# Kernel tuning notes

Hardware: AMD Instinct MI355X
Metric: run time of the kernel (lower is better)

The kernel has to match this reference:

```python
import jax, jax.numpy as jnp
import numpy as np

H = 4            # attention heads
N = 50000        # num nodes
E = 800000       # num edges
IN, HID, OUT = 256, 32, 32
NEG_SLOPE = 0.2  # DGL GATConv default leaky_relu slope


def setup_inputs() -> dict:
    key = jax.random.key(0)
    ks = jax.random.split(key, 16)
    x = jax.random.normal(ks[0], (N, IN), jnp.float32)
    src = jax.random.randint(ks[1], (E,), 0, N, dtype=jnp.int32)
    dst = jax.random.randint(ks[2], (E,), 0, N, dtype=jnp.int32)

    def lin(k, a, b):
        return jax.random.normal(k, (a, b), jnp.float32) * (1.0 / np.sqrt(a))

    def attn(k, d):
        return jax.random.normal(k, (H, d), jnp.float32) * 0.1

    HW = H * HID
    return {
        "x": x, "src": src, "dst": dst,
        "W1": lin(ks[3], IN, HW), "al1": attn(ks[4], HID), "ar1": attn(ks[5], HID), "b1": jnp.zeros((H, HID), jnp.float32),
        "W2": lin(ks[6], HW, HW), "al2": attn(ks[7], HID), "ar2": attn(ks[8], HID), "b2": jnp.zeros((H, HID), jnp.float32),
        "W3": lin(ks[9], HW, H * OUT), "al3": attn(ks[10], OUT), "ar3": attn(ks[11], OUT), "b3": jnp.zeros((H, OUT), jnp.float32),
    }


def gat_layer(x, W, al, ar, b, src, dst, act):
    # x: [N, F_in]; W: [F_in, H*D]; al/ar/b: [H, D]
    n = x.shape[0]
    d = al.shape[1]
    h = (x @ W).reshape(n, H, d)                         # [N, H, D]
    el = jnp.sum(h * al, axis=-1)                        # [N, H]
    er = jnp.sum(h * ar, axis=-1)                        # [N, H]
    e = jax.nn.leaky_relu(el[src] + er[dst], NEG_SLOPE)  # [E, H] edge scores
    # segment softmax over incoming edges of each dst node
    m = jax.ops.segment_max(e, dst, num_segments=n)      # [N, H]
    m = jnp.where(jnp.isfinite(m), m, 0.0)               # empty segments -> -inf
    ex = jnp.exp(e - m[dst])                             # [E, H]
    s = jax.ops.segment_sum(ex, dst, num_segments=n)     # [N, H]
    alpha = ex / s[dst]                                  # [E, H]
    out = jax.ops.segment_sum(h[src] * alpha[:, :, None], dst, num_segments=n)  # [N, H, D]
    out = out + b
    return act(out) if act is not None else out


def reference(x, src, dst, W1, al1, ar1, b1, W2, al2, ar2, b2, W3, al3, ar3, b3):
    h = gat_layer(x, W1, al1, ar1, b1, src, dst, jax.nn.relu).reshape(N, -1)   # flatten heads
    h = gat_layer(h, W2, al2, ar2, b2, src, dst, jax.nn.elu).reshape(N, -1)    # flatten heads
    h = gat_layer(h, W3, al3, ar3, b3, src, dst, None).mean(axis=1)            # mean over heads
    return h
```

## Files before the change

### kernel.cpp

```cpp
#include <hip/hip_runtime.h>
#include <hip/hip_bf16.h>
#include <hip/hip_fp16.h>
#include <stdint.h>

#define NNODES 50000
#define NEDGES 800000
#define HEADS 4
#define DSTRIDE 64

#define GEMM_GRID ((NNODES + 127) / 128)
#define B2_GROUPS 8
#define B2_PER_GROUP 256
#define NODES_PER_GROUP (NNODES / B2_GROUPS)

typedef __attribute__((ext_vector_type(8))) short bf16x8;
typedef __attribute__((ext_vector_type(4))) float f32x4;

union frag_u { uint32_t u[4]; bf16x8 v; uint4 q; };

__device__ __forceinline__ float lrelu(float x) { return x > 0.f ? x : 0.2f * x; }

__device__ __forceinline__ uint32_t pack_bf16(float a, float b) {
  __hip_bfloat162 t{__float2bfloat16(a), __float2bfloat16(b)};
  return *reinterpret_cast<uint32_t*>(&t);
}

__device__ __forceinline__ void split8(const float4& x0, const float4& x1,
                                       frag_u& hi, frag_u& lo) {
  float f[8] = {x0.x, x0.y, x0.z, x0.w, x1.x, x1.y, x1.z, x1.w};
#pragma unroll
  for (int p = 0; p < 4; ++p) {
    uint32_t ua = __float_as_uint(f[2 * p]);
    uint32_t ub = __float_as_uint(f[2 * p + 1]);
    hi.u[p] = (ua >> 16) | (ub & 0xffff0000u);
    float ra = f[2 * p] - __uint_as_float(ua & 0xffff0000u);
    float rb = f[2 * p + 1] - __uint_as_float(ub & 0xffff0000u);
    lo.u[p] = (__float_as_uint(ra) >> 16) | (__float_as_uint(rb) & 0xffff0000u);
  }
}

__global__ __launch_bounds__(256) void k_build2(const int* __restrict__ src,
                                                const int* __restrict__ dst,
                                                int* __restrict__ cnt,
                                                unsigned short* __restrict__ esrc) {
  int g = blockIdx.x & (B2_GROUPS - 1);
  int sub = blockIdx.x >> 3;
  int lo = g * NODES_PER_GROUP, hi = lo + NODES_PER_GROUP;
  const int tstride = B2_PER_GROUP * 256 * 8;
  for (int e = (sub * 256 + threadIdx.x) * 8; e < NEDGES; e += tstride) {
    int4 da = *(const int4*)&dst[e];
    int4 db = *(const int4*)&dst[e + 4];
#pragma unroll
    for (int q = 0; q < 8; ++q) {
      int d = q < 4 ? (q == 0 ? da.x : q == 1 ? da.y : q == 2 ? da.z : da.w)
                    : (q == 4 ? db.x : q == 5 ? db.y : q == 6 ? db.z : db.w);
      if (d >= lo && d < hi) {
        int r = atomicAdd(&cnt[d], 1);
        if (r < DSTRIDE) esrc[(size_t)d * DSTRIDE + r] = (unsigned short)src[e + q];
      }
    }
  }
}

__device__ __forceinline__ void splitw_one(const float* __restrict__ W, int t_local,
                                           uint4* __restrict__ WPh, uint4* __restrict__ WPl) {
  int lane = t_local & 63;
  int ct = (t_local >> 6) & 7;
  int ks = t_local >> 9;
  int lg = lane >> 4, lm = lane & 15;
  int n = ct * 16 + lm;
  frag_u hi, lo;
#pragma unroll
  for (int p = 0; p < 4; ++p) {
    float a = W[(size_t)(ks * 32 + lg * 8 + 2 * p) * 128 + n];
    float b = W[(size_t)(ks * 32 + lg * 8 + 2 * p + 1) * 128 + n];
    uint32_t ua = __float_as_uint(a), ub = __float_as_uint(b);
    hi.u[p] = (ua >> 16) | (ub & 0xffff0000u);
    float ra = a - __uint_as_float(ua & 0xffff0000u);
    float rb = b - __uint_as_float(ub & 0xffff0000u);
    lo.u[p] = (__float_as_uint(ra) >> 16) | (__float_as_uint(rb) & 0xffff0000u);
  }
  WPh[t_local] = hi.q;
  WPl[t_local] = lo.q;
}

__global__ void k_splitw_all(const float* __restrict__ W1, const float* __restrict__ W2,
                             const float* __restrict__ W3,
                             uint4* __restrict__ WPh1, uint4* __restrict__ WPl1,
                             uint4* __restrict__ WPh2, uint4* __restrict__ WPl2,
                             uint4* __restrict__ WPh3, uint4* __restrict__ WPl3,
                             int* __restrict__ cnt) {
  int t = blockIdx.x * blockDim.x + threadIdx.x;
  for (int i = t; i < NNODES; i += 32 * 256) cnt[i] = 0;
  int ks = t >> 9;
  if (ks < 8)        splitw_one(W1, t,            WPh1, WPl1);
  else if (ks < 12)  splitw_one(W2, t - 8 * 512,  WPh2, WPl2);
  else if (ks < 16)  splitw_one(W3, t - 12 * 512, WPh3, WPl3);
}

template <int K, int XBF>
__global__ __launch_bounds__(256) void k_gemm_mfma(
    const void* __restrict__ Xv, const uint4* __restrict__ WPh,
    const uint4* __restrict__ WPl, const float* __restrict__ al,
    const float* __restrict__ ar, uint32_t* __restrict__ Hb,
    float* __restrict__ el, float* __restrict__ er, int nrows) {
  __shared__ uint4 lph[512];
  __shared__ uint4 lpl[512];
  const int tid = threadIdx.x;
  const int wv = tid >> 6;
  const int lane = tid & 63;
  const int lm = lane & 15;
  const int lg = lane >> 4;
  const int rbase = blockIdx.x * 128 + wv * 32;

  int grow0 = rbase + lm;
  int grow1 = rbase + 16 + lm;
  int lrow0 = min(grow0, nrows - 1);
  int lrow1 = min(grow1, nrows - 1);

  const float* xp0 = nullptr;
  const float* xp1 = nullptr;
  const uint32_t* xq0 = nullptr;
  const uint32_t* xq1 = nullptr;
  if (XBF) {
    xq0 = (const uint32_t*)Xv + (size_t)lrow0 * 64 + lg * 4;
    xq1 = (const uint32_t*)Xv + (size_t)lrow1 * 64 + lg * 4;
  } else {
    xp0 = (const float*)Xv + (size_t)lrow0 * K + lg * 8;
    xp1 = (const float*)Xv + (size_t)lrow1 * K + lg * 8;
  }

  f32x4 acc[2][8];
#pragma unroll
  for (int rt = 0; rt < 2; ++rt)
#pragma unroll
    for (int ct = 0; ct < 8; ++ct) acc[rt][ct] = f32x4{0.f, 0.f, 0.f, 0.f};

  for (int ks = 0; ks < K / 32; ++ks) {
    frag_u xh0, xl0, xh1, xl1;
    if (XBF) {
      xh0.q = *(const uint4*)(xq0 + ks * 16);
      xh1.q = *(const uint4*)(xq1 + ks * 16);
    } else {
      float4 a0 = *(const float4*)(xp0 + ks * 32);
      float4 a1 = *(const float4*)(xp0 + ks * 32 + 4);
      float4 b0 = *(const float4*)(xp1 + ks * 32);
      float4 b1 = *(const float4*)(xp1 + ks * 32 + 4);
      split8(a0, a1, xh0, xl0);
      split8(b0, b1, xh1, xl1);
    }
    lph[tid]       = WPh[(size_t)ks * 512 + tid];
    lph[tid + 256] = WPh[(size_t)ks * 512 + 256 + tid];
    lpl[tid]       = WPl[(size_t)ks * 512 + tid];
    lpl[tid + 256] = WPl[(size_t)ks * 512 + 256 + tid];
    __syncthreads();
#pragma unroll
    for (int ct = 0; ct < 8; ++ct) {
      frag_u bh, bl;
      bh.q = lph[ct * 64 + lane];
      bl.q = lpl[ct * 64 + lane];
      if (XBF) {
        acc[0][ct] = __builtin_amdgcn_mfma_f32_16x16x32_bf16(bh.v, xh0.v, acc[0][ct], 0, 0, 0);
        acc[0][ct] = __builtin_amdgcn_mfma_f32_16x16x32_bf16(bl.v, xh0.v, acc[0][ct], 0, 0, 0);
        acc[1][ct] = __builtin_amdgcn_mfma_f32_16x16x32_bf16(bh.v, xh1.v, acc[1][ct], 0, 0, 0);
        acc[1][ct] = __builtin_amdgcn_mfma_f32_16x16x32_bf16(bl.v, xh1.v, acc[1][ct], 0, 0, 0);
      } else {
        acc[0][ct] = __builtin_amdgcn_mfma_f32_16x16x32_bf16(bh.v, xh0.v, acc[0][ct], 0, 0, 0);
        acc[0][ct] = __builtin_amdgcn_mfma_f32_16x16x32_bf16(bl.v, xh0.v, acc[0][ct], 0, 0, 0);
        acc[0][ct] = __builtin_amdgcn_mfma_f32_16x16x32_bf16(bh.v, xl0.v, acc[0][ct], 0, 0, 0);
        acc[1][ct] = __builtin_amdgcn_mfma_f32_16x16x32_bf16(bh.v, xh1.v, acc[1][ct], 0, 0, 0);
        acc[1][ct] = __builtin_amdgcn_mfma_f32_16x16x32_bf16(bl.v, xh1.v, acc[1][ct], 0, 0, 0);
        acc[1][ct] = __builtin_amdgcn_mfma_f32_16x16x32_bf16(bh.v, xl1.v, acc[1][ct], 0, 0, 0);
      }
    }
    __syncthreads();
  }

#pragma unroll
  for (int rt = 0; rt < 2; ++rt) {
    int grow = rt ? grow1 : grow0;
    float pe[4] = {0.f, 0.f, 0.f, 0.f};
    float pr[4] = {0.f, 0.f, 0.f, 0.f};
#pragma unroll
    for (int ct = 0; ct < 8; ++ct) {
      int h = ct >> 1;
      int dc = (ct & 1) * 16 + lg * 4;
      float4 a4 = *(const float4*)&al[h * 32 + dc];
      float4 r4 = *(const float4*)&ar[h * 32 + dc];
      f32x4 c = acc[rt][ct];
      pe[h] += c[0] * a4.x + c[1] * a4.y + c[2] * a4.z + c[3] * a4.w;
      pr[h] += c[0] * r4.x + c[1] * r4.y + c[2] * r4.z + c[3] * r4.w;
    }
#pragma unroll
    for (int i = 0; i < 4; ++i) {
      pe[i] += __shfl_xor(pe[i], 16); pe[i] += __shfl_xor(pe[i], 32);
      pr[i] += __shfl_xor(pr[i], 16); pr[i] += __shfl_xor(pr[i], 32);
    }
    if (grow < nrows) {
#pragma unroll
      for (int ct = 0; ct < 8; ++ct) {
        f32x4 c = acc[rt][ct];
        uint2 st{pack_bf16(c[0], c[1]), pack_bf16(c[2], c[3])};
        *(uint2*)&Hb[(size_t)grow * 64 + ct * 8 + lg * 2] = st;
      }
      if (lg == 0) {
        *(float4*)&el[(size_t)grow * 4] = float4{pe[0], pe[1], pe[2], pe[3]};
        *(float4*)&er[(size_t)grow * 4] = float4{pr[0], pr[1], pr[2], pr[3]};
      }
    }
  }
}

template <int MODE>
__global__ __launch_bounds__(256) void k_agg(const uint32_t* __restrict__ Hb,
                                             const float* __restrict__ el,
                                             const float* __restrict__ er,
                                             const int* __restrict__ deg_,
                                             const unsigned short* __restrict__ esrc,
                                             const float* __restrict__ B,
                                             void* __restrict__ outp) {
  int gt = blockIdx.x * blockDim.x + threadIdx.x;
  int v = gt >> 6;
  int lane = gt & 63;
  if (v >= NNODES) return;
  int deg = min(deg_[v], DSTRIDE);
  int h = lane >> 4;
  int e16 = lane & 15;
  float erh = er[(size_t)v * 4 + h];
  const int vbase = v * DSTRIDE;

  float den = 0.f, acc0 = 0.f, acc1 = 0.f;
  for (int base = 0; base < deg; base += 16) {
    uint32_t pk = 0;
    if (base + e16 < deg) {
      int u = esrc[vbase + base + e16];
      float ex1 = __expf(lrelu(el[(size_t)u * 4 + h] + erh));
      den += ex1;
      pk = ((uint32_t)u << 16) | (uint32_t)__half_as_ushort(__float2half(ex1));
    }
    uint32_t hw[16];
    float w[16];
#pragma unroll
    for (int j = 0; j < 16; ++j) {
      int srcl = (lane & 48) | j;
      uint32_t pkj = __shfl(pk, srcl);
      w[j] = __half2float(__ushort_as_half((unsigned short)(pkj & 0xffffu)));
      hw[j] = Hb[(size_t)(pkj >> 16) * 64 + lane];
    }
#pragma unroll
    for (int j = 0; j < 16; ++j) {
      acc0 += w[j] * __uint_as_float(hw[j] << 16);
      acc1 += w[j] * __uint_as_float(hw[j] & 0xffff0000u);
    }
  }
#pragma unroll
  for (int s = 1; s < 16; s <<= 1) den += __shfl_xor(den, s);
  float inv = den > 0.f ? 1.f / den : 0.f;

  int d = (2 * lane) & 31;
  float v0 = acc0 * inv + B[h * 32 + d];
  float v1 = acc1 * inv + B[h * 32 + d + 1];

  if (MODE == 0) {
    ((uint32_t*)outp)[(size_t)v * 64 + lane] = pack_bf16(fmaxf(v0, 0.f), fmaxf(v1, 0.f));
  } else if (MODE == 1) {
    float a0 = v0 > 0.f ? v0 : expm1f(v0);
    float a1 = v1 > 0.f ? v1 : expm1f(v1);
    ((uint32_t*)outp)[(size_t)v * 64 + lane] = pack_bf16(a0, a1);
  } else {
    float t0 = v0, t1 = v1;
    t0 += __shfl_xor(t0, 16); t0 += __shfl_xor(t0, 32);
    t1 += __shfl_xor(t1, 16); t1 += __shfl_xor(t1, 32);
    if (lane < 16) {
      float2 o{t0 * 0.25f, t1 * 0.25f};
      *(float2*)((float*)outp + (size_t)v * 32 + 2 * lane) = o;
    }
  }
}

extern "C" void kernel_launch(void* const* d_in, const int* in_sizes, int n_in,
                              void* d_out, int out_size, void* d_ws, size_t ws_size,
                              hipStream_t stream) {
  const float* x   = (const float*)d_in[0];
  const int* src   = (const int*)d_in[1];
  const int* dst   = (const int*)d_in[2];
  const float* W1  = (const float*)d_in[3];
  const float* al1 = (const float*)d_in[4];
  const float* ar1 = (const float*)d_in[5];
  const float* b1  = (const float*)d_in[6];
  const float* W2  = (const float*)d_in[7];
  const float* al2 = (const float*)d_in[8];
  const float* ar2 = (const float*)d_in[9];
  const float* b2  = (const float*)d_in[10];
  const float* W3  = (const float*)d_in[11];
  const float* al3 = (const float*)d_in[12];
  const float* ar3 = (const float*)d_in[13];
  const float* b3  = (const float*)d_in[14];

  uint8_t* p = (uint8_t*)d_ws;
  auto alloc = [&](size_t bytes) {
    uint8_t* r = p;
    p += (bytes + 255) & ~(size_t)255;
    return r;
  };
  uint32_t* Hb          = (uint32_t*)alloc((size_t)NNODES * 64 * 4);
  uint32_t* Ab          = (uint32_t*)alloc((size_t)NNODES * 64 * 4);
  float* el             = (float*)alloc((size_t)NNODES * 4 * 4);
  float* er             = (float*)alloc((size_t)NNODES * 4 * 4);
  int* cnt              = (int*)alloc((size_t)NNODES * 4);
  unsigned short* esrc  = (unsigned short*)alloc((size_t)NNODES * DSTRIDE * 2);
  uint4* WPh1           = (uint4*)alloc((size_t)256 * 16 * 16);
  uint4* WPl1           = (uint4*)alloc((size_t)256 * 16 * 16);
  uint4* WPh2           = (uint4*)alloc((size_t)128 * 16 * 16);
  uint4* WPl2           = (uint4*)alloc((size_t)128 * 16 * 16);
  uint4* WPh3           = (uint4*)alloc((size_t)128 * 16 * 16);
  uint4* WPl3           = (uint4*)alloc((size_t)128 * 16 * 16);

  k_splitw_all<<<32, 256, 0, stream>>>(W1, W2, W3, WPh1, WPl1, WPh2, WPl2,
                                       WPh3, WPl3, cnt);
  k_build2<<<B2_GROUPS * B2_PER_GROUP, 256, 0, stream>>>(src, dst, cnt, esrc);

  const int agg_grid = (NNODES * 64 + 255) / 256;

  k_gemm_mfma<256, 0><<<GEMM_GRID, 256, 0, stream>>>(x, WPh1, WPl1, al1, ar1, Hb, el, er, NNODES);
  k_agg<0><<<agg_grid, 256, 0, stream>>>(Hb, el, er, cnt, esrc, b1, Ab);

  k_gemm_mfma<128, 1><<<GEMM_GRID, 256, 0, stream>>>(Ab, WPh2, WPl2, al2, ar2, Hb, el, er, NNODES);
  k_agg<1><<<agg_grid, 256, 0, stream>>>(Hb, el, er, cnt, esrc, b2, Ab);

  k_gemm_mfma<128, 1><<<GEMM_GRID, 256, 0, stream>>>(Ab, WPh3, WPl3, al3, ar3, Hb, el, er, NNODES);
  k_agg<2><<<agg_grid, 256, 0, stream>>>(Hb, el, er, cnt, esrc, b3, d_out);
}
```

Baseline: 215.1 us.

## Replace group-filtered edge scan with two-pass bucket partition for CSR build

The adjacency build used to scan every edge eight times, once per destination-node group, so each group's atomics stayed localized. It now runs a single bucketing pass that packs (local dst, src) into 32-bit entries and appends them to per-group buckets, using shared-memory counts and one global atomic per block per group. A second kernel then scatters each bucket into the per-node esrc slots. This removes the repeated full reads of dst, but adds an intermediate buffer with a fixed capacity per group that could overflow on skewed inputs, and an extra kernel launch.

```diff
diff --git a/kernel.cpp b/kernel.cpp
--- a/kernel.cpp
+++ b/kernel.cpp
@@ -9,9 +9,10 @@
 #define DSTRIDE 64
 
 #define GEMM_GRID ((NNODES + 127) / 128)
-#define B2_GROUPS 8
-#define B2_PER_GROUP 256
-#define NODES_PER_GROUP (NNODES / B2_GROUPS)
+#define NGROUPS 8
+#define GROUP_SHIFT 13
+#define BUCK_CAP 163840
+#define SC2_BPG 128
 
 typedef __attribute__((ext_vector_type(8))) short bf16x8;
 typedef __attribute__((ext_vector_type(4))) float f32x4;
@@ -39,25 +40,61 @@
   }
 }
 
-__global__ __launch_bounds__(256) void k_build2(const int* __restrict__ src,
+__global__ __launch_bounds__(256) void k_bucket(const int* __restrict__ src,
                                                 const int* __restrict__ dst,
-                                                int* __restrict__ cnt,
-                                                unsigned short* __restrict__ esrc) {
-  int g = blockIdx.x & (B2_GROUPS - 1);
+                                                int* __restrict__ bcnt,
+                                                uint32_t* __restrict__ bucket) {
+  __shared__ int lcnt[NGROUPS], lbase[NGROUPS];
+  if (threadIdx.x < NGROUPS) lcnt[threadIdx.x] = 0;
+  __syncthreads();
+  int e0 = (blockIdx.x * 256 + threadIdx.x) * 4;
+  int g[4], rank[4];
+  uint32_t entry[4];
+  int4 d4, s4;
+  if (e0 < NEDGES) {
+    d4 = *(const int4*)&dst[e0];
+    s4 = *(const int4*)&src[e0];
+  }
+#pragma unroll
+  for (int q = 0; q < 4; ++q) {
+    if (e0 < NEDGES) {
+      int d = q == 0 ? d4.x : q == 1 ? d4.y : q == 2 ? d4.z : d4.w;
+      int s = q == 0 ? s4.x : q == 1 ? s4.y : q == 2 ? s4.z : s4.w;
+      g[q] = d >> GROUP_SHIFT;
+      entry[q] = ((uint32_t)(d & ((1 << GROUP_SHIFT) - 1)) << 16) | (uint32_t)s;
+      rank[q] = atomicAdd(&lcnt[g[q]], 1);
+    } else {
+      g[q] = -1;
+    }
+  }
+  __syncthreads();
+  if (threadIdx.x < NGROUPS && lcnt[threadIdx.x] > 0)
+    lbase[threadIdx.x] = atomicAdd(&bcnt[threadIdx.x], lcnt[threadIdx.x]);
+  __syncthreads();
+#pragma unroll
+  for (int q = 0; q < 4; ++q) {
+    if (g[q] >= 0) {
+      uint32_t pos = (uint32_t)(lbase[g[q]] + rank[q]);
+      if (pos < BUCK_CAP) bucket[(size_t)g[q] * BUCK_CAP + pos] = entry[q];
+    }
+  }
+}
+
+__global__ __launch_bounds__(256) void k_scatter2(const int* __restrict__ bcnt,
+                                                  const uint32_t* __restrict__ bucket,
+                                                  int* __restrict__ cnt,
+                                                  unsigned short* __restrict__ esrc) {
+  int g = blockIdx.x & (NGROUPS - 1);
   int sub = blockIdx.x >> 3;
-  int lo = g * NODES_PER_GROUP, hi = lo + NODES_PER_GROUP;
-  const int tstride = B2_PER_GROUP * 256 * 8;
-  for (int e = (sub * 256 + threadIdx.x) * 8; e < NEDGES; e += tstride) {
-    int4 da = *(const int4*)&dst[e];
-    int4 db = *(const int4*)&dst[e + 4];
-#pragma unroll
-    for (int q = 0; q < 8; ++q) {
-      int d = q < 4 ? (q == 0 ? da.x : q == 1 ? da.y : q == 2 ? da.z : da.w)
-                    : (q == 4 ? db.x : q == 5 ? db.y : q == 6 ? db.z : db.w);
-      if (d >= lo && d < hi) {
-        int r = atomicAdd(&cnt[d], 1);
-        if (r < DSTRIDE) esrc[(size_t)d * DSTRIDE + r] = (unsigned short)src[e + q];
-      }
+  int n = min(bcnt[g], BUCK_CAP);
+  const uint32_t* bk = bucket + (size_t)g * BUCK_CAP;
+  int gbase = g << GROUP_SHIFT;
+  for (int i = sub * 256 + threadIdx.x; i < n; i += SC2_BPG * 256) {
+    uint32_t ent = bk[i];
+    int d = gbase + (int)(ent >> 16);
+    if (d < NNODES) {
+      int r = atomicAdd(&cnt[d], 1);
+      if (r < DSTRIDE) esrc[(size_t)d * DSTRIDE + r] = (unsigned short)(ent & 0xffffu);
     }
   }
 }
@@ -89,9 +126,10 @@
                              uint4* __restrict__ WPh1, uint4* __restrict__ WPl1,
                              uint4* __restrict__ WPh2, uint4* __restrict__ WPl2,
                              uint4* __restrict__ WPh3, uint4* __restrict__ WPl3,
-                             int* __restrict__ cnt) {
+                             int* __restrict__ cnt, int* __restrict__ bcnt) {
   int t = blockIdx.x * blockDim.x + threadIdx.x;
   for (int i = t; i < NNODES; i += 32 * 256) cnt[i] = 0;
+  if (t < NGROUPS) bcnt[t] = 0;
   int ks = t >> 9;
   if (ks < 8)        splitw_one(W1, t,            WPh1, WPl1);
   else if (ks < 12)  splitw_one(W2, t - 8 * 512,  WPh2, WPl2);
@@ -309,6 +347,8 @@
   float* er             = (float*)alloc((size_t)NNODES * 4 * 4);
   int* cnt              = (int*)alloc((size_t)NNODES * 4);
   unsigned short* esrc  = (unsigned short*)alloc((size_t)NNODES * DSTRIDE * 2);
+  int* bcnt             = (int*)alloc(NGROUPS * 4);
+  uint32_t* bucket      = (uint32_t*)alloc((size_t)NGROUPS * BUCK_CAP * 4);
   uint4* WPh1           = (uint4*)alloc((size_t)256 * 16 * 16);
   uint4* WPl1           = (uint4*)alloc((size_t)256 * 16 * 16);
   uint4* WPh2           = (uint4*)alloc((size_t)128 * 16 * 16);
@@ -317,8 +357,9 @@
   uint4* WPl3           = (uint4*)alloc((size_t)128 * 16 * 16);
 
   k_splitw_all<<<32, 256, 0, stream>>>(W1, W2, W3, WPh1, WPl1, WPh2, WPl2,
-                                       WPh3, WPl3, cnt);
-  k_build2<<<B2_GROUPS * B2_PER_GROUP, 256, 0, stream>>>(src, dst, cnt, esrc);
+                                       WPh3, WPl3, cnt, bcnt);
+  k_bucket<<<(NEDGES / 4 + 255) / 256, 256, 0, stream>>>(src, dst, bcnt, bucket);
+  k_scatter2<<<NGROUPS * SC2_BPG, 256, 0, stream>>>(bcnt, bucket, cnt, esrc);
 
   const int agg_grid = (NNODES * 64 + 255) / 256;
 
```

New measurement: 224.3 us. +4.3%, slower.
